# Kernel tuning notes

Hardware: AMD Instinct MI355X
Metric: run time of the kernel (lower is better)

The kernel has to match this reference:

```python
import jax, jax.numpy as jnp
import numpy as np
import math

# static config
NH, HD, HID = 16, 128, 2048
ROT = 64            # head_dim * partial_rotary_factor(0.5)
EPS = 1e-6
GROUPS = 8
CHUNK = 64
THETA = 10000.0
LAYER_IDX, N_LAYERS = 1, 32
B, S = 2, 2048


def _base_slopes(n):
    # power-of-two branch of HF ALiBi slopes
    start = 2 ** (-(2 ** (-(math.log2(n) - 3))))
    return [start * (start ** i) for i in range(n)]

# per-head log-decay (negative): slope = -base * (1 - (l-1)/(L-1) + 1e-5)
SLOPE = jnp.asarray(
    -np.array(_base_slopes(NH), dtype=np.float32)
    * (1.0 - (LAYER_IDX - 1) / (N_LAYERS - 1) + 1e-5),
    dtype=jnp.float32)  # [NH]


def _rmsnorm(x, w):
    return x * jax.lax.rsqrt(jnp.mean(x * x, axis=-1, keepdims=True) + EPS) * w


def _partial_rope(x, positions):
    # x: [B,S,NH,HD]; neox-style rotary on first ROT dims, rest passthrough
    half = ROT // 2
    inv_freq = 1.0 / (THETA ** (jnp.arange(half, dtype=jnp.float32) / half))
    ang = positions.astype(jnp.float32)[:, None] * inv_freq       # [S, half]
    cos = jnp.cos(ang)[None, :, None, :]
    sin = jnp.sin(ang)[None, :, None, :]
    x1, x2, rest = x[..., :half], x[..., half:ROT], x[..., ROT:]
    return jnp.concatenate(
        [x1 * cos - x2 * sin, x2 * cos + x1 * sin, rest], axis=-1)


def setup_inputs() -> dict:
    key = jax.random.key(0)
    ks = jax.random.split(key, 4)
    return {
        'positions': jnp.arange(S, dtype=jnp.int32),
        'hidden_states': jax.random.normal(ks[0], (B, S, HID), jnp.float32),
        'recurrent_state': jnp.zeros((B, NH, HD, HD), jnp.float32),
        'w_qkv': jax.random.normal(ks[1], (HID, 3 * NH * HD), jnp.float32) * 0.02,
        'w_g': jax.random.normal(ks[2], (HID, NH * HD), jnp.float32) * 0.02,
        'w_dense': jax.random.normal(ks[3], (NH * HD, HID), jnp.float32) * 0.02,
        'q_norm_w': jnp.ones((HD,), jnp.float32),
        'k_norm_w': jnp.ones((HD,), jnp.float32),
        'g_norm_w': jnp.ones((NH * HD,), jnp.float32),
    }


def reference(positions, hidden_states, recurrent_state, w_qkv, w_g, w_dense,
              q_norm_w, k_norm_w, g_norm_w):
    # fused QKV projection
    qkv = hidden_states @ w_qkv                       # [B,S,3*NH*HD]
    q, k, v = jnp.split(qkv, 3, axis=-1)
    q = q.reshape(B, S, NH, HD)
    k = k.reshape(B, S, NH, HD)
    v = v.reshape(B, S, NH, HD)

    # QK RMSNorm then partial rotary
    q = _partial_rope(_rmsnorm(q, q_norm_w), positions)
    k = _partial_rope(_rmsnorm(k, k_norm_w), positions)

    # chunked ALiBi-decayed linear attention:
    #   S_t = lam * S_{t-1} + k_t v_t^T ; o_t = q_t S_t, lam = exp(slope)
    NC = S // CHUNK
    qc = q.reshape(B, NC, CHUNK, NH, HD).transpose(1, 0, 3, 2, 4)  # [NC,B,NH,C,HD]
    kc = k.reshape(B, NC, CHUNK, NH, HD).transpose(1, 0, 3, 2, 4)
    vc = v.reshape(B, NC, CHUNK, NH, HD).transpose(1, 0, 3, 2, 4)

    t = jnp.arange(CHUNK, dtype=jnp.float32)
    # intra-chunk causal decay mask lam^(i-j), i>=j: [NH,C,C]
    dec_mask = jnp.where(t[:, None] >= t[None, :],
                         jnp.exp(SLOPE[:, None, None] * (t[:, None] - t[None, :])),
                         0.0)
    q_dec = jnp.exp(SLOPE[:, None] * (t[None, :] + 1.0))            # [NH,C] lam^(i+1)
    k_dec = jnp.exp(SLOPE[:, None] * (CHUNK - 1.0 - t[None, :]))    # [NH,C] lam^(C-1-j)
    lam_C = jnp.exp(SLOPE * CHUNK)                                   # [NH]

    def step(state, inp):
        qb, kb, vb = inp                                  # [B,NH,C,HD]
        scores = jnp.einsum('bhid,bhjd->bhij', qb, kb) * dec_mask[None]
        o_intra = jnp.einsum('bhij,bhjd->bhid', scores, vb)
        o_inter = jnp.einsum('bhid,bhde->bhie', qb * q_dec[None, :, :, None], state)
        new_state = (state * lam_C[None, :, None, None]
                     + jnp.einsum('bhjd,bhje->bhde', kb * k_dec[None, :, :, None], vb))
        return new_state, o_intra + o_inter

    _, o = jax.lax.scan(step, recurrent_state, (qc, kc, vc))  # o: [NC,B,NH,C,HD]
    o = o.transpose(1, 0, 3, 2, 4).reshape(B, S, NH * HD)

    # GroupRMSNorm on attention output, sigmoid gate, output projection
    og = o.reshape(B, S, GROUPS, (NH * HD) // GROUPS)
    og = og * jax.lax.rsqrt(jnp.mean(og * og, axis=-1, keepdims=True) + EPS)
    o = og.reshape(B, S, NH * HD) * g_norm_w
    o = o * jax.nn.sigmoid(hidden_states @ w_g)
    return o @ w_dense
```

## Files before the change

kernel.cpp:

```cpp
#include <hip/hip_runtime.h>
#include <hip/hip_bf16.h>
#include <math.h>

#define NH   16
#define HD   128
#define HID  2048
#define NKV  6144
#define B_   2
#define S_   2048
#define NC   32
#define CHUNK_ 64
#define GROUPS_ 8

typedef __bf16 bf16_t;
typedef bf16_t bf16x8 __attribute__((ext_vector_type(8)));
typedef float  f32x4  __attribute__((ext_vector_type(4)));

__device__ __forceinline__ float b2f(unsigned int u) {
    union { unsigned int u; float f; } c; c.u = (u & 0xffffu) << 16; return c.f;
}
__device__ __forceinline__ unsigned int f2b(float f) {
    union { float f; unsigned int u; } c; c.f = f;
    unsigned int u = c.u;
    return (u + 0x7fffu + ((u >> 16) & 1u)) >> 16;
}

#define GLOAD_LDS16(gp, lp) __builtin_amdgcn_global_load_lds(                     \
    (const __attribute__((address_space(1))) void*)(gp),                          \
    (__attribute__((address_space(3))) void*)(lp), 16, 0, 0)

__global__ __launch_bounds__(256) void cvt_bf16(const float* __restrict__ in,
                                                unsigned short* __restrict__ out, int n8)
{
    int i = blockIdx.x * 256 + threadIdx.x;
    if (i >= n8) return;
    const float4* p = (const float4*)in + (size_t)i * 2;
    float4 a = p[0], b = p[1];
    uint4 o;
    o.x = f2b(a.x) | (f2b(a.y) << 16);
    o.y = f2b(a.z) | (f2b(a.w) << 16);
    o.z = f2b(b.x) | (f2b(b.y) << 16);
    o.w = f2b(b.z) | (f2b(b.w) << 16);
    ((uint4*)out)[i] = o;
}

__global__ __launch_bounds__(256) void transpose_cvt(const float* __restrict__ in,
                                                     unsigned short* __restrict__ out,
                                                     int Kdim, int Ndim)
{
    __shared__ float tile[32][33];
    int ntx = Ndim >> 5;
    int bx = blockIdx.x % ntx;
    int by = blockIdx.x / ntx;
    int lx = threadIdx.x & 31, ly = threadIdx.x >> 5;
    int r0 = by * 32, c0 = bx * 32;
    #pragma unroll
    for (int r = 0; r < 4; ++r)
        tile[ly + r * 8][lx] = in[(size_t)(r0 + ly + r * 8) * Ndim + c0 + lx];
    __syncthreads();
    #pragma unroll
    for (int r = 0; r < 4; ++r)
        out[(size_t)(c0 + ly + r * 8) * Kdim + r0 + lx] = (unsigned short)f2b(tile[lx][ly + r * 8]);
}


__device__ __forceinline__ void ld_fr4(bf16x8 (&d)[4][2], const bf16_t* b, int s0, int ri) {
    #pragma unroll
    for (int i = 0; i < 4; ++i)
        #pragma unroll
        for (int k = 0; k < 2; ++k)
            d[i][k] = *(const bf16x8*)(b + (((s0 + i) * 2 + k) << 9) + ri);
}
__device__ __forceinline__ void ld_fr2(bf16x8 (&d)[2][2], const bf16_t* b, int s0, int ri) {
    #pragma unroll
    for (int i = 0; i < 2; ++i)
        #pragma unroll
        for (int k = 0; k < 2; ++k)
            d[i][k] = *(const bf16x8*)(b + (((s0 + i) * 2 + k) << 9) + ri);
}
__device__ __forceinline__ void mfma_quad(f32x4 (&a)[4][2], const bf16x8 (&af)[4][2],
                                          const bf16x8 (&bv)[2][2]) {
    #pragma unroll
    for (int mt = 0; mt < 4; ++mt)
        #pragma unroll
        for (int nt = 0; nt < 2; ++nt)
            #pragma unroll
            for (int ks = 0; ks < 2; ++ks)
                a[mt][nt] = __builtin_amdgcn_mfma_f32_16x16x32_bf16(af[mt][ks], bv[nt][ks], a[mt][nt], 0, 0, 0);
}

#define BAR()     asm volatile("s_barrier" ::: "memory")
#define VMCNT0()  asm volatile("s_waitcnt vmcnt(0)" ::: "memory")

__global__ __launch_bounds__(512, 2) void gemm_qg_256(const bf16_t* __restrict__ A,
                                                      const bf16_t* __restrict__ Bt,
                                                      unsigned short* __restrict__ Cq,
                                                      unsigned short* __restrict__ Cg)
{
    __shared__ bf16_t Asm[2][2][8192];
    __shared__ bf16_t Bsm[2][2][8192];
    const int K  = HID;
    const int NT = K / 64;

    int tid  = threadIdx.x;
    int wave = tid >> 6, lane = tid & 63;
    int wm = wave >> 2, wn = wave & 3;
    int l16 = lane & 15, quad = lane >> 4;
    int wm4 = wm * 4, wn2 = wn * 2;

    int bid = blockIdx.x;
    int xcd = bid & 7, idx = bid >> 3;
    int by  = (xcd >> 2) * 8 + (idx >> 3);
    int bx  = (xcd & 3) * 8 + (idx & 7);

    int rd_in = ((l16 << 5) | (quad << 3)) ^ (((l16 >> 3) & 1) << 4);

    int ch = lane ^ ((lane & 32) >> 4);
    int rr = ch >> 2;
    int cc = (ch & 3) * 8;

    const bf16_t* aSrc0 = A  + (size_t)(by * 256 +       wave * 16 + rr) * K + cc;
    const bf16_t* aSrc1 = A  + (size_t)(by * 256 + 128 + wave * 16 + rr) * K + cc;
    const bf16_t* bSrc0 = Bt + (size_t)(bx * 256 +       wave * 16 + rr) * K + cc;
    const bf16_t* bSrc1 = Bt + (size_t)(bx * 256 + 128 + wave * 16 + rr) * K + cc;

#define STAGE_A(h, t) do {                                                        \
        const bf16_t* _g = ((h) ? aSrc1 : aSrc0) + (size_t)(t) * 64;              \
        bf16_t* _l = &Asm[(t) & 1][(h)][wave * 1024 + lane * 8];                  \
        GLOAD_LDS16(_g,      _l);                                                 \
        GLOAD_LDS16(_g + 32, _l + 512); } while (0)
#define STAGE_B(h, t) do {                                                        \
        const bf16_t* _g = ((h) ? bSrc1 : bSrc0) + (size_t)(t) * 64;              \
        bf16_t* _l = &Bsm[(t) & 1][(h)][wave * 1024 + lane * 8];                  \
        GLOAD_LDS16(_g,      _l);                                                 \
        GLOAD_LDS16(_g + 32, _l + 512); } while (0)

    f32x4 acc[2][2][4][2];
    #pragma unroll
    for (int a0 = 0; a0 < 2; ++a0)
        #pragma unroll
        for (int a1 = 0; a1 < 2; ++a1)
            #pragma unroll
            for (int a2 = 0; a2 < 4; ++a2)
                #pragma unroll
                for (int a3 = 0; a3 < 2; ++a3) { f32x4 z = {0.f,0.f,0.f,0.f}; acc[a0][a1][a2][a3] = z; }

    STAGE_A(0, 0); STAGE_B(0, 0); STAGE_A(1, 0); STAGE_B(1, 0);
    VMCNT0();
    BAR();

    #pragma unroll 2
    for (int t = 0; t < NT - 1; ++t) {
        const int buf = t & 1;
        STAGE_A(0, t + 1); STAGE_B(0, t + 1); STAGE_A(1, t + 1); STAGE_B(1, t + 1);
        {
            bf16x8 afA[4][2], afB[4][2], bf0[2][2], bf1[2][2];
            ld_fr4(afA, &Asm[buf][0][0], wm4, rd_in);
            ld_fr2(bf0, &Bsm[buf][0][0], wn2, rd_in);
            mfma_quad(acc[0][0], afA, bf0);
            ld_fr2(bf1, &Bsm[buf][1][0], wn2, rd_in);
            mfma_quad(acc[0][1], afA, bf1);
            ld_fr4(afB, &Asm[buf][1][0], wm4, rd_in);
            mfma_quad(acc[1][1], afB, bf1);
            mfma_quad(acc[1][0], afB, bf0);
        }
        VMCNT0();
        BAR();
    }
    {
        const int buf = (NT - 1) & 1;
        bf16x8 afA[4][2], afB[4][2], bf0[2][2], bf1[2][2];
        ld_fr4(afA, &Asm[buf][0][0], wm4, rd_in);
        ld_fr2(bf0, &Bsm[buf][0][0], wn2, rd_in);
        mfma_quad(acc[0][0], afA, bf0);
        ld_fr2(bf1, &Bsm[buf][1][0], wn2, rd_in);
        mfma_quad(acc[0][1], afA, bf1);
        ld_fr4(afB, &Asm[buf][1][0], wm4, rd_in);
        mfma_quad(acc[1][1], afB, bf1);
        mfma_quad(acc[1][0], afB, bf0);
    }
#undef STAGE_A
#undef STAGE_B

    unsigned short* Cc; int Nn, colbase;
    if (bx < 24) { Cc = Cq; Nn = NKV; colbase = bx * 256; }
    else         { Cc = Cg; Nn = HID; colbase = bx * 256 - NKV; }
    int row0 = by * 256 + wm * 64 + quad * 4;
    int col0 = colbase + wn * 32 + l16;
    #pragma unroll
    for (int mh = 0; mh < 2; ++mh)
        #pragma unroll
        for (int nh = 0; nh < 2; ++nh)
            #pragma unroll
            for (int mt = 0; mt < 4; ++mt)
                #pragma unroll
                for (int nt = 0; nt < 2; ++nt) {
                    int col = col0 + nh * 128 + nt * 16;
                    #pragma unroll
                    for (int r = 0; r < 4; ++r) {
                        int row = row0 + mh * 128 + mt * 16 + r;
                        Cc[(size_t)row * Nn + col] = (unsigned short)f2b(acc[mh][nh][mt][nt][r]);
                    }
                }
}

__global__ __launch_bounds__(256, 2) void gemm_out_128(const bf16_t* __restrict__ A,
                                                       const bf16_t* __restrict__ Bt,
                                                       float* __restrict__ C)
{
    __shared__ bf16_t As[2][4096];
    __shared__ bf16_t Bs[2][4096];
    const int K  = HID;
    const int NT = K / 32;

    int tid  = threadIdx.x;
    int wave = tid >> 6, lane = tid & 63;
    int wm2 = wave >> 1, wn2 = wave & 1;
    int l16 = lane & 15, quad = lane >> 4;
    int w2 = wave * 2;

    int bid = blockIdx.x;
    int xcd = bid & 7, idx = bid >> 3;
    int by  = (xcd >> 1) * 8 + (idx >> 3);
    int bx  = (xcd & 1) * 8 + (idx & 7);

    int rd_in = ((l16 << 5) | (quad << 3)) ^ (((l16 >> 3) & 1) << 4);
    int ch = lane ^ ((lane & 32) >> 4);
    int rr = ch >> 2;
    int cc = (ch & 3) * 8;

    const bf16_t* aSrc = A  + (size_t)(by * 128 + w2 * 16 + rr) * K + cc;
    const bf16_t* bSrc = Bt + (size_t)(bx * 128 + w2 * 16 + rr) * K + cc;

#define OSTAGE(t) do {                                                            \
        const int nb_ = (t) & 1;                                                  \
        const bf16_t* _ga = aSrc + (size_t)(t) * 32;                              \
        const bf16_t* _gb = bSrc + (size_t)(t) * 32;                              \
        GLOAD_LDS16(_ga,                  &As[nb_][w2 * 512 + lane * 8]);         \
        GLOAD_LDS16(_ga + (size_t)16 * K, &As[nb_][w2 * 512 + 512 + lane * 8]);   \
        GLOAD_LDS16(_gb,                  &Bs[nb_][w2 * 512 + lane * 8]);         \
        GLOAD_LDS16(_gb + (size_t)16 * K, &Bs[nb_][w2 * 512 + 512 + lane * 8]); } while (0)

    f32x4 acc[4][4];
    #pragma unroll
    for (int i = 0; i < 4; ++i)
        #pragma unroll
        for (int j = 0; j < 4; ++j) { f32x4 z = {0.f,0.f,0.f,0.f}; acc[i][j] = z; }

#define OCOMP(t) do {                                                             \
        const int b_ = (t) & 1;                                                   \
        bf16x8 af_[4], bf_[4];                                                    \
        _Pragma("unroll")                                                         \
        for (int i = 0; i < 4; ++i)                                               \
            af_[i] = *(const bf16x8*)(&As[b_][((wm2 * 4 + i) << 9) + rd_in]);     \
        _Pragma("unroll")                                                         \
        for (int j = 0; j < 4; ++j)                                               \
            bf_[j] = *(const bf16x8*)(&Bs[b_][((wn2 * 4 + j) << 9) + rd_in]);     \
        _Pragma("unroll")                                                         \
        for (int i = 0; i < 4; ++i)                                               \
            _Pragma("unroll")                                                     \
            for (int j = 0; j < 4; ++j)                                           \
                acc[i][j] = __builtin_amdgcn_mfma_f32_16x16x32_bf16(af_[i], bf_[j], acc[i][j], 0, 0, 0); } while (0)

    OSTAGE(0);
    VMCNT0();
    BAR();
    #pragma unroll 2
    for (int t = 0; t < NT - 1; ++t) {
        OSTAGE(t + 1);
        OCOMP(t);
        VMCNT0();
        BAR();
    }
    OCOMP(NT - 1);
#undef OSTAGE
#undef OCOMP

    #pragma unroll
    for (int i = 0; i < 4; ++i)
        #pragma unroll
        for (int j = 0; j < 4; ++j) {
            int col = bx * 128 + wn2 * 64 + j * 16 + l16;
            #pragma unroll
            for (int r = 0; r < 4; ++r) {
                int row = by * 128 + wm2 * 64 + i * 16 + quad * 4 + r;
                C[(size_t)row * HID + col] = acc[i][j][r];
            }
        }
}

__global__ __launch_bounds__(256) void norm_rope(unsigned short* __restrict__ qkv,
                                                 const int* __restrict__ positions,
                                                 const float* __restrict__ qw,
                                                 const float* __restrict__ kw)
{
    int bs = blockIdx.x;
    int s  = bs & (S_ - 1);
    int tid = threadIdx.x;
    int l16 = tid & 15;
    unsigned short* base = qkv + (size_t)bs * NKV;
    float pos = (float)positions[s];

    #pragma unroll
    for (int p = 0; p < 2; ++p) {
        int rr = p * 16 + (tid >> 4);
        int qk = rr >> 4;
        int h  = rr & 15;
        unsigned short* row = base + qk * HID + h * HD;
        const float* w = qk ? kw : qw;
        uint4 v = *(const uint4*)(row + l16 * 8);
        float x[8];
        x[0] = b2f(v.x); x[1] = b2f(v.x >> 16);
        x[2] = b2f(v.y); x[3] = b2f(v.y >> 16);
        x[4] = b2f(v.z); x[5] = b2f(v.z >> 16);
        x[6] = b2f(v.w); x[7] = b2f(v.w >> 16);
        float ss = 0.f;
        #pragma unroll
        for (int t = 0; t < 8; ++t) ss += x[t] * x[t];
        ss += __shfl_xor(ss, 1); ss += __shfl_xor(ss, 2);
        ss += __shfl_xor(ss, 4); ss += __shfl_xor(ss, 8);
        float inv = rsqrtf(ss * (1.0f / 128.0f) + 1e-6f);
        float n[8];
        #pragma unroll
        for (int t = 0; t < 8; ++t) n[t] = x[t] * inv * w[l16 * 8 + t];
        float pr[8];
        #pragma unroll
        for (int t = 0; t < 8; ++t) pr[t] = __shfl_xor(n[t], 4);
        if (l16 < 8) {
            #pragma unroll
            for (int t = 0; t < 8; ++t) {
                int dim = l16 * 8 + t;
                int i = dim & 31;
                float ang = pos * exp2f(-(float)i * 0.4152410118609203f);
                float cs = cosf(ang), sn = sinf(ang);
                n[t] = (dim < 32) ? (n[t] * cs - pr[t] * sn) : (n[t] * cs + pr[t] * sn);
            }
        }
        uint4 o;
        o.x = f2b(n[0]) | (f2b(n[1]) << 16);
        o.y = f2b(n[2]) | (f2b(n[3]) << 16);
        o.z = f2b(n[4]) | (f2b(n[5]) << 16);
        o.w = f2b(n[6]) | (f2b(n[7]) << 16);
        *(uint4*)(row + l16 * 8) = o;
    }
}

__global__ __launch_bounds__(256) void chunk_kv(const unsigned short* __restrict__ qkv,
                                                unsigned short* __restrict__ wbuf)
{
    __shared__ unsigned short kt[128 * 72];
    __shared__ unsigned short vt[128 * 72];
    int bi = blockIdx.x;
    int c = bi & 31, bh = bi >> 5, h = bh & 15, b = bh >> 4;
    int tid = threadIdx.x;
    float slope = -exp2f(-0.5f * (float)(h + 1)) * (1.0f + 1e-5f);

    const unsigned short* kbase = qkv + ((size_t)(b * S_ + c * CHUNK_)) * NKV + HID + h * HD;
    const unsigned short* vbase = kbase + HID;

    for (int idx = tid; idx < 4096; idx += 256) {
        int j = idx >> 6, p = idx & 63;
        unsigned int ku = *(const unsigned int*)(kbase + (size_t)j * NKV + p * 2);
        kt[(2 * p) * 72 + j]     = (unsigned short)(ku & 0xffffu);
        kt[(2 * p + 1) * 72 + j] = (unsigned short)(ku >> 16);
        float kd = expf(slope * (float)(63 - j));
        unsigned int vu = *(const unsigned int*)(vbase + (size_t)j * NKV + p * 2);
        vt[(2 * p) * 72 + j]     = (unsigned short)f2b(b2f(vu) * kd);
        vt[(2 * p + 1) * 72 + j] = (unsigned short)f2b(b2f(vu >> 16) * kd);
    }
    __syncthreads();

    int lane = tid & 63, wave = tid >> 6;
    int wm = (wave >> 1) * 64;
    int wn = (wave & 1) * 64;
    int l16 = lane & 15, quad = lane >> 4;

    f32x4 acc[4][4];
    #pragma unroll
    for (int i = 0; i < 4; ++i)
        #pragma unroll
        for (int j = 0; j < 4; ++j) { f32x4 z = {0.f,0.f,0.f,0.f}; acc[i][j] = z; }

    #pragma unroll
    for (int ks = 0; ks < 64; ks += 32) {
        bf16x8 af[4], bf[4];
        #pragma unroll
        for (int t = 0; t < 4; ++t) {
            af[t] = *(const bf16x8*)((const bf16_t*)vt + (wm + t * 16 + l16) * 72 + ks + quad * 8);
            bf[t] = *(const bf16x8*)((const bf16_t*)kt + (wn + t * 16 + l16) * 72 + ks + quad * 8);
        }
        #pragma unroll
        for (int mt = 0; mt < 4; ++mt)
            #pragma unroll
            for (int nt = 0; nt < 4; ++nt)
                acc[mt][nt] = __builtin_amdgcn_mfma_f32_16x16x32_bf16(af[mt], bf[nt], acc[mt][nt], 0, 0, 0);
    }

    unsigned short* wp = wbuf + ((size_t)bi << 14);
    #pragma unroll
    for (int mt = 0; mt < 4; ++mt)
        #pragma unroll
        for (int nt = 0; nt < 4; ++nt) {
            int dcol = wn + nt * 16 + l16;
            #pragma unroll
            for (int r = 0; r < 4; ++r) {
                int erow = wm + mt * 16 + quad * 4 + r;
                wp[(size_t)erow * 128 + dcol] = (unsigned short)f2b(acc[mt][nt][r]);
            }
        }
}

__global__ __launch_bounds__(256) void state_scan(const unsigned short* __restrict__ wbuf,
                                                  const float* __restrict__ rs0,
                                                  unsigned short* __restrict__ stbuf)
{
    int bi = blockIdx.x;
    int es = bi & 15, bh = bi >> 4, h = bh & 15, b = bh >> 4;
    int tid = threadIdx.x;
    float slope = -exp2f(-0.5f * (float)(h + 1)) * (1.0f + 1e-5f);
    float lam = expf(slope * 64.0f);

    int e  = es * 8 + (tid >> 5);
    int d0 = (tid & 31) * 4;

    float S[4];
    const float* rp = rs0 + ((size_t)(b * NH + h)) * HD * HD + e;
    #pragma unroll
    for (int t = 0; t < 4; ++t) S[t] = rp[(size_t)(d0 + t) * HD];

    size_t off = (size_t)e * 128 + d0;
    size_t base = (((size_t)bh * NC) << 14) + off;
    uint2 w0 = *(const uint2*)(wbuf + base);
    uint2 w1 = *(const uint2*)(wbuf + base + (1 << 14));
    for (int c = 0; c < NC; ++c) {
        uint2 o;
        o.x = f2b(S[0]) | (f2b(S[1]) << 16);
        o.y = f2b(S[2]) | (f2b(S[3]) << 16);
        *(uint2*)(stbuf + base) = o;
        uint2 w2 = w1;
        if (c + 2 < NC) w2 = *(const uint2*)(wbuf + base + (2 << 14));
        S[0] = S[0] * lam + b2f(w0.x);
        S[1] = S[1] * lam + b2f(w0.x >> 16);
        S[2] = S[2] * lam + b2f(w0.y);
        S[3] = S[3] * lam + b2f(w0.y >> 16);
        w0 = w1; w1 = w2;
        base += (1 << 14);
    }
}

__global__ __launch_bounds__(256) void chunk_out(const unsigned short* __restrict__ qkv,
                                                 const unsigned short* __restrict__ stbuf,
                                                 unsigned short* __restrict__ obuf)
{
    __shared__ unsigned short qs[64 * 136];
    __shared__ unsigned short kss[64 * 136];
    __shared__ unsigned short vt[128 * 72];
    __shared__ unsigned short sc[64 * 72];

    int bi = blockIdx.x;
    int c = bi & 31, bh = bi >> 5, h = bh & 15, b = bh >> 4;
    int tid = threadIdx.x;
    float slope = -exp2f(-0.5f * (float)(h + 1)) * (1.0f + 1e-5f);

    int lane = tid & 63, wave = tid >> 6;
    int l16 = lane & 15, quad = lane >> 4;
    int wn3 = wave * 32;

    const unsigned short* stp = stbuf + (((size_t)bh * NC + c) << 14);
    bf16x8 bsf[4][2];
    #pragma unroll
    for (int ksp4 = 0; ksp4 < 4; ++ksp4)
        #pragma unroll
        for (int nt = 0; nt < 2; ++nt)
            bsf[ksp4][nt] = *(const bf16x8*)((const bf16_t*)stp +
                (size_t)(wn3 + nt * 16 + l16) * 128 + ksp4 * 32 + quad * 8);

    const unsigned short* qrow = qkv + ((size_t)(b * S_ + c * CHUNK_)) * NKV + h * HD;
    const unsigned short* krow = qrow + HID;
    for (int idx = tid; idx < 1024; idx += 256) {
        int row = idx >> 4, c8 = (idx & 15) * 8;
        *(uint4*)(qs  + row * 136 + c8) = *(const uint4*)(qrow + (size_t)row * NKV + c8);
        *(uint4*)(kss + row * 136 + c8) = *(const uint4*)(krow + (size_t)row * NKV + c8);
    }
    const unsigned short* vbase = qrow + 2 * HID;
    for (int idx = tid; idx < 4096; idx += 256) {
        int j = idx >> 6, p = idx & 63;
        unsigned int vu = *(const unsigned int*)(vbase + (size_t)j * NKV + p * 2);
        vt[(2 * p) * 72 + j]     = (unsigned short)(vu & 0xffffu);
        vt[(2 * p + 1) * 72 + j] = (unsigned short)(vu >> 16);
    }
    __syncthreads();

    {
        f32x4 accS[4];
        #pragma unroll
        for (int t = 0; t < 4; ++t) { f32x4 z = {0.f,0.f,0.f,0.f}; accS[t] = z; }
        #pragma unroll
        for (int ksp = 0; ksp < 128; ksp += 32) {
            bf16x8 aq = *(const bf16x8*)((const bf16_t*)qs + (wave * 16 + l16) * 136 + ksp + quad * 8);
            #pragma unroll
            for (int nt = 0; nt < 4; ++nt) {
                bf16x8 bk = *(const bf16x8*)((const bf16_t*)kss + (nt * 16 + l16) * 136 + ksp + quad * 8);
                accS[nt] = __builtin_amdgcn_mfma_f32_16x16x32_bf16(aq, bk, accS[nt], 0, 0, 0);
            }
        }
        float ad[4];
        #pragma unroll
        for (int r = 0; r < 4; ++r) ad[r] = expf(slope * (float)(wave * 16 + quad * 4 + r));
        #pragma unroll
        for (int nt = 0; nt < 4; ++nt) {
            int j = nt * 16 + l16;
            float bd = expf(-slope * (float)j);
            #pragma unroll
            for (int r = 0; r < 4; ++r) {
                int i = wave * 16 + quad * 4 + r;
                float v = (i >= j) ? accS[nt][r] * ad[r] * bd : 0.0f;
                sc[i * 72 + j] = (unsigned short)f2b(v);
            }
        }
    }
    __syncthreads();

    f32x4 accI[4][2], accE[4][2];
    #pragma unroll
    for (int i = 0; i < 4; ++i)
        #pragma unroll
        for (int j = 0; j < 2; ++j) { f32x4 z = {0.f,0.f,0.f,0.f}; accI[i][j] = z; accE[i][j] = z; }

    #pragma unroll
    for (int ksp = 0; ksp < 64; ksp += 32) {
        bf16x8 as[4], bv[2];
        #pragma unroll
        for (int mt = 0; mt < 4; ++mt)
            as[mt] = *(const bf16x8*)((const bf16_t*)sc + (mt * 16 + l16) * 72 + ksp + quad * 8);
        #pragma unroll
        for (int nt = 0; nt < 2; ++nt)
            bv[nt] = *(const bf16x8*)((const bf16_t*)vt + (wn3 + nt * 16 + l16) * 72 + ksp + quad * 8);
        #pragma unroll
        for (int mt = 0; mt < 4; ++mt)
            #pragma unroll
            for (int nt = 0; nt < 2; ++nt)
                accI[mt][nt] = __builtin_amdgcn_mfma_f32_16x16x32_bf16(as[mt], bv[nt], accI[mt][nt], 0, 0, 0);
    }
    #pragma unroll
    for (int ksp4 = 0; ksp4 < 4; ++ksp4) {
        bf16x8 aq[4];
        #pragma unroll
        for (int mt = 0; mt < 4; ++mt)
            aq[mt] = *(const bf16x8*)((const bf16_t*)qs + (mt * 16 + l16) * 136 + ksp4 * 32 + quad * 8);
        #pragma unroll
        for (int mt = 0; mt < 4; ++mt)
            #pragma unroll
            for (int nt = 0; nt < 2; ++nt)
                accE[mt][nt] = __builtin_amdgcn_mfma_f32_16x16x32_bf16(aq[mt], bsf[ksp4][nt], accE[mt][nt], 0, 0, 0);
    }

    #pragma unroll
    for (int mt = 0; mt < 4; ++mt) {
        #pragma unroll
        for (int r = 0; r < 4; ++r) {
            int i = mt * 16 + quad * 4 + r;
            float qd = expf(slope * (float)(i + 1));
            int orow = b * S_ + c * CHUNK_ + i;
            #pragma unroll
            for (int nt = 0; nt < 2; ++nt) {
                int col = h * HD + wn3 + nt * 16 + l16;
                float o = accI[mt][nt][r] + qd * accE[mt][nt][r];
                obuf[(size_t)orow * 2048 + col] = (unsigned short)f2b(o);
            }
        }
    }
}

__global__ __launch_bounds__(256) void gnorm_gate(const unsigned short* __restrict__ o,
                                                  unsigned short* __restrict__ gate,
                                                  const float* __restrict__ gw)
{
    int row = blockIdx.x >> 3;
    int g   = blockIdx.x & 7;
    int col = g * 256 + threadIdx.x;
    size_t idx = (size_t)row * 2048 + col;
    float ov = b2f(o[idx]);
    float ss = ov * ov;
    #pragma unroll
    for (int off = 32; off > 0; off >>= 1) ss += __shfl_xor(ss, off);
    __shared__ float part[4];
    if ((threadIdx.x & 63) == 0) part[threadIdx.x >> 6] = ss;
    __syncthreads();
    float tot = part[0] + part[1] + part[2] + part[3];
    float inv = rsqrtf(tot * (1.0f / 256.0f) + 1e-6f);
    float gv = b2f(gate[idx]);
    float sig = 1.0f / (1.0f + expf(-gv));
    gate[idx] = (unsigned short)f2b(ov * inv * gw[col] * sig);
}

extern "C" void kernel_launch(void* const* d_in, const int* in_sizes, int n_in,
                              void* d_out, int out_size, void* d_ws, size_t ws_size,
                              hipStream_t stream) {
    const int*   positions = (const int*)d_in[0];
    const float* hidden    = (const float*)d_in[1];
    const float* rstate    = (const float*)d_in[2];
    const float* w_qkv     = (const float*)d_in[3];
    const float* w_g       = (const float*)d_in[4];
    const float* w_dense   = (const float*)d_in[5];
    const float* q_norm_w  = (const float*)d_in[6];
    const float* k_norm_w  = (const float*)d_in[7];
    const float* g_norm_w  = (const float*)d_in[8];
    float* out = (float*)d_out;

    const int MR = B_ * S_;

    char* w = (char*)d_ws;
    unsigned short* qkv  = (unsigned short*)w;            w += (size_t)MR * NKV * 2;
    unsigned short* gbuf = (unsigned short*)w;            w += (size_t)MR * 2048 * 2;
    unsigned short* wdT  = (unsigned short*)w;            w += (size_t)HID * HID * 2;
    char* regionA = w;                                    w += (size_t)MR * HID * 2 + (size_t)8192 * HID * 2;
    char* regionB = w;
    unsigned short* hbf   = (unsigned short*)regionA;
    unsigned short* btQG  = (unsigned short*)(regionA + (size_t)MR * HID * 2);
    unsigned short* wqT   = btQG;
    unsigned short* wgT   = btQG + (size_t)NKV * HID;
    unsigned short* stbuf = (unsigned short*)regionA;
    unsigned short* wbuf  = (unsigned short*)regionB;
    unsigned short* obuf  = (unsigned short*)regionB;

    cvt_bf16<<<dim3((MR * HID / 8 + 255) / 256), dim3(256), 0, stream>>>(hidden, hbf, MR * HID / 8);
    transpose_cvt<<<dim3((HID / 32) * (NKV / 32)), dim3(256), 0, stream>>>(w_qkv, wqT, HID, NKV);
    transpose_cvt<<<dim3((HID / 32) * (HID / 32)), dim3(256), 0, stream>>>(w_g, wgT, HID, HID);
    transpose_cvt<<<dim3((HID / 32) * (HID / 32)), dim3(256), 0, stream>>>(w_dense, wdT, HID, HID);

    gemm_qg_256<<<dim3(512), dim3(512), 0, stream>>>(
        (const bf16_t*)hbf, (const bf16_t*)btQG, qkv, gbuf);
    norm_rope<<<dim3(B_ * S_), dim3(256), 0, stream>>>(qkv, positions, q_norm_w, k_norm_w);

    chunk_kv<<<dim3(B_ * NH * NC), dim3(256), 0, stream>>>(qkv, wbuf);
    state_scan<<<dim3(B_ * NH * 16), dim3(256), 0, stream>>>(wbuf, rstate, stbuf);
    chunk_out<<<dim3(B_ * NH * NC), dim3(256), 0, stream>>>(qkv, stbuf, obuf);

    gnorm_gate<<<dim3(MR * GROUPS_), dim3(256), 0, stream>>>(obuf, gbuf, g_norm_w);
    gemm_out_128<<<dim3(512), dim3(256), 0, stream>>>(
        (const bf16_t*)gbuf, (const bf16_t*)wdT, out);
}
```

Before: 424.1 us.

## Retile QG GEMM to 128x256, fragment-native state layout, vectorize scan and gnorm

The QKV/gate GEMM drops from 256x256 tiles with 512 threads to 128x256 tiles with 256 threads, K-step 32, launched over 1024 blocks. The state buffer is now written in MFMA-fragment order so chunk_out can read B fragments with contiguous per-lane loads. state_scan is changed to 8-element vectors to match. gnorm_gate now handles one full row per block with 8 bf16 values per thread and reduces with wave shuffles. These changes aim to cut GEMM tail and occupancy costs and uncoalesced memory access, at the price of lower per-block reuse in the GEMM and a layout that must agree across three kernels.

Result: slower. 435.6 us (+2.7%).

```diff
diff --git a/kernel.cpp b/kernel.cpp
--- a/kernel.cpp
+++ b/kernel.cpp
@@ -28,6 +28,9 @@
 #define GLOAD_LDS16(gp, lp) __builtin_amdgcn_global_load_lds(                     \
     (const __attribute__((address_space(1))) void*)(gp),                          \
     (__attribute__((address_space(3))) void*)(lp), 16, 0, 0)
+
+#define BAR()     asm volatile("s_barrier" ::: "memory")
+#define VMCNT0()  asm volatile("s_waitcnt vmcnt(0)" ::: "memory")
 
 __global__ __launch_bounds__(256) void cvt_bf16(const float* __restrict__ in,
                                                 unsigned short* __restrict__ out, int n8)
@@ -63,145 +66,93 @@
         out[(size_t)(c0 + ly + r * 8) * Kdim + r0 + lx] = (unsigned short)f2b(tile[lx][ly + r * 8]);
 }
 
-
-__device__ __forceinline__ void ld_fr4(bf16x8 (&d)[4][2], const bf16_t* b, int s0, int ri) {
-    #pragma unroll
-    for (int i = 0; i < 4; ++i)
-        #pragma unroll
-        for (int k = 0; k < 2; ++k)
-            d[i][k] = *(const bf16x8*)(b + (((s0 + i) * 2 + k) << 9) + ri);
-}
-__device__ __forceinline__ void ld_fr2(bf16x8 (&d)[2][2], const bf16_t* b, int s0, int ri) {
-    #pragma unroll
-    for (int i = 0; i < 2; ++i)
-        #pragma unroll
-        for (int k = 0; k < 2; ++k)
-            d[i][k] = *(const bf16x8*)(b + (((s0 + i) * 2 + k) << 9) + ri);
-}
-__device__ __forceinline__ void mfma_quad(f32x4 (&a)[4][2], const bf16x8 (&af)[4][2],
-                                          const bf16x8 (&bv)[2][2]) {
-    #pragma unroll
-    for (int mt = 0; mt < 4; ++mt)
-        #pragma unroll
-        for (int nt = 0; nt < 2; ++nt)
-            #pragma unroll
-            for (int ks = 0; ks < 2; ++ks)
-                a[mt][nt] = __builtin_amdgcn_mfma_f32_16x16x32_bf16(af[mt][ks], bv[nt][ks], a[mt][nt], 0, 0, 0);
-}
-
-#define BAR()     asm volatile("s_barrier" ::: "memory")
-#define VMCNT0()  asm volatile("s_waitcnt vmcnt(0)" ::: "memory")
-
-__global__ __launch_bounds__(512, 2) void gemm_qg_256(const bf16_t* __restrict__ A,
+__global__ __launch_bounds__(256, 2) void gemm_qg_128(const bf16_t* __restrict__ A,
                                                       const bf16_t* __restrict__ Bt,
                                                       unsigned short* __restrict__ Cq,
                                                       unsigned short* __restrict__ Cg)
 {
-    __shared__ bf16_t Asm[2][2][8192];
-    __shared__ bf16_t Bsm[2][2][8192];
+    __shared__ bf16_t Asm[2][4096];
+    __shared__ bf16_t Bsm[2][8192];
     const int K  = HID;
-    const int NT = K / 64;
+    const int NT = K / 32;
 
     int tid  = threadIdx.x;
     int wave = tid >> 6, lane = tid & 63;
-    int wm = wave >> 2, wn = wave & 3;
     int l16 = lane & 15, quad = lane >> 4;
-    int wm4 = wm * 4, wn2 = wn * 2;
 
     int bid = blockIdx.x;
     int xcd = bid & 7, idx = bid >> 3;
-    int by  = (xcd >> 2) * 8 + (idx >> 3);
-    int bx  = (xcd & 3) * 8 + (idx & 7);
+    int by  = (xcd >> 1) * 8 + (idx >> 4);
+    int bx  = (xcd & 1) * 16 + (idx & 15);
 
     int rd_in = ((l16 << 5) | (quad << 3)) ^ (((l16 >> 3) & 1) << 4);
-
     int ch = lane ^ ((lane & 32) >> 4);
     int rr = ch >> 2;
     int cc = (ch & 3) * 8;
 
-    const bf16_t* aSrc0 = A  + (size_t)(by * 256 +       wave * 16 + rr) * K + cc;
-    const bf16_t* aSrc1 = A  + (size_t)(by * 256 + 128 + wave * 16 + rr) * K + cc;
-    const bf16_t* bSrc0 = Bt + (size_t)(bx * 256 +       wave * 16 + rr) * K + cc;
-    const bf16_t* bSrc1 = Bt + (size_t)(bx * 256 + 128 + wave * 16 + rr) * K + cc;
-
-#define STAGE_A(h, t) do {                                                        \
-        const bf16_t* _g = ((h) ? aSrc1 : aSrc0) + (size_t)(t) * 64;              \
-        bf16_t* _l = &Asm[(t) & 1][(h)][wave * 1024 + lane * 8];                  \
-        GLOAD_LDS16(_g,      _l);                                                 \
-        GLOAD_LDS16(_g + 32, _l + 512); } while (0)
-#define STAGE_B(h, t) do {                                                        \
-        const bf16_t* _g = ((h) ? bSrc1 : bSrc0) + (size_t)(t) * 64;              \
-        bf16_t* _l = &Bsm[(t) & 1][(h)][wave * 1024 + lane * 8];                  \
-        GLOAD_LDS16(_g,      _l);                                                 \
-        GLOAD_LDS16(_g + 32, _l + 512); } while (0)
-
-    f32x4 acc[2][2][4][2];
-    #pragma unroll
-    for (int a0 = 0; a0 < 2; ++a0)
-        #pragma unroll
-        for (int a1 = 0; a1 < 2; ++a1)
-            #pragma unroll
-            for (int a2 = 0; a2 < 4; ++a2)
-                #pragma unroll
-                for (int a3 = 0; a3 < 2; ++a3) { f32x4 z = {0.f,0.f,0.f,0.f}; acc[a0][a1][a2][a3] = z; }
-
-    STAGE_A(0, 0); STAGE_B(0, 0); STAGE_A(1, 0); STAGE_B(1, 0);
+    const bf16_t* aSrc = A  + (size_t)(by * 128 + wave * 32 + rr) * K + cc;
+    const bf16_t* bSrc = Bt + (size_t)(bx * 256 + wave * 64 + rr) * K + cc;
+
+#define QSTAGE(t) do {                                                            \
+        const int nb_ = (t) & 1;                                                  \
+        const bf16_t* _ga = aSrc + (size_t)(t) * 32;                              \
+        const bf16_t* _gb = bSrc + (size_t)(t) * 32;                              \
+        GLOAD_LDS16(_ga,                  &Asm[nb_][(2*wave  )*512 + lane*8]);    \
+        GLOAD_LDS16(_ga + (size_t)16 * K, &Asm[nb_][(2*wave+1)*512 + lane*8]);    \
+        GLOAD_LDS16(_gb,                  &Bsm[nb_][(4*wave  )*512 + lane*8]);    \
+        GLOAD_LDS16(_gb + (size_t)16 * K, &Bsm[nb_][(4*wave+1)*512 + lane*8]);    \
+        GLOAD_LDS16(_gb + (size_t)32 * K, &Bsm[nb_][(4*wave+2)*512 + lane*8]);    \
+        GLOAD_LDS16(_gb + (size_t)48 * K, &Bsm[nb_][(4*wave+3)*512 + lane*8]); } while (0)
+
+    f32x4 acc[8][4];
+    #pragma unroll
+    for (int i = 0; i < 8; ++i)
+        #pragma unroll
+        for (int j = 0; j < 4; ++j) { f32x4 z = {0.f,0.f,0.f,0.f}; acc[i][j] = z; }
+
+#define QCOMP(t) do {                                                             \
+        const int b_ = (t) & 1;                                                   \
+        bf16x8 af_[8], bf_[4];                                                    \
+        _Pragma("unroll")                                                         \
+        for (int j = 0; j < 4; ++j)                                               \
+            bf_[j] = *(const bf16x8*)(&Bsm[b_][((wave*4 + j) << 9) + rd_in]);     \
+        _Pragma("unroll")                                                         \
+        for (int i = 0; i < 8; ++i)                                               \
+            af_[i] = *(const bf16x8*)(&Asm[b_][(i << 9) + rd_in]);                \
+        _Pragma("unroll")                                                         \
+        for (int i = 0; i < 8; ++i)                                               \
+            _Pragma("unroll")                                                     \
+            for (int j = 0; j < 4; ++j)                                           \
+                acc[i][j] = __builtin_amdgcn_mfma_f32_16x16x32_bf16(af_[i], bf_[j], acc[i][j], 0, 0, 0); } while (0)
+
+    QSTAGE(0);
     VMCNT0();
     BAR();
-
     #pragma unroll 2
     for (int t = 0; t < NT - 1; ++t) {
-        const int buf = t & 1;
-        STAGE_A(0, t + 1); STAGE_B(0, t + 1); STAGE_A(1, t + 1); STAGE_B(1, t + 1);
-        {
-            bf16x8 afA[4][2], afB[4][2], bf0[2][2], bf1[2][2];
-            ld_fr4(afA, &Asm[buf][0][0], wm4, rd_in);
-            ld_fr2(bf0, &Bsm[buf][0][0], wn2, rd_in);
-            mfma_quad(acc[0][0], afA, bf0);
-            ld_fr2(bf1, &Bsm[buf][1][0], wn2, rd_in);
-            mfma_quad(acc[0][1], afA, bf1);
-            ld_fr4(afB, &Asm[buf][1][0], wm4, rd_in);
-            mfma_quad(acc[1][1], afB, bf1);
-            mfma_quad(acc[1][0], afB, bf0);
-        }
+        QSTAGE(t + 1);
+        QCOMP(t);
         VMCNT0();
         BAR();
     }
-    {
-        const int buf = (NT - 1) & 1;
-        bf16x8 afA[4][2], afB[4][2], bf0[2][2], bf1[2][2];
-        ld_fr4(afA, &Asm[buf][0][0], wm4, rd_in);
-        ld_fr2(bf0, &Bsm[buf][0][0], wn2, rd_in);
-        mfma_quad(acc[0][0], afA, bf0);
-        ld_fr2(bf1, &Bsm[buf][1][0], wn2, rd_in);
-        mfma_quad(acc[0][1], afA, bf1);
-        ld_fr4(afB, &Asm[buf][1][0], wm4, rd_in);
-        mfma_quad(acc[1][1], afB, bf1);
-        mfma_quad(acc[1][0], afB, bf0);
-    }
-#undef STAGE_A
-#undef STAGE_B
+    QCOMP(NT - 1);
+#undef QSTAGE
+#undef QCOMP
 
     unsigned short* Cc; int Nn, colbase;
     if (bx < 24) { Cc = Cq; Nn = NKV; colbase = bx * 256; }
     else         { Cc = Cg; Nn = HID; colbase = bx * 256 - NKV; }
-    int row0 = by * 256 + wm * 64 + quad * 4;
-    int col0 = colbase + wn * 32 + l16;
-    #pragma unroll
-    for (int mh = 0; mh < 2; ++mh)
-        #pragma unroll
-        for (int nh = 0; nh < 2; ++nh)
-            #pragma unroll
-            for (int mt = 0; mt < 4; ++mt)
-                #pragma unroll
-                for (int nt = 0; nt < 2; ++nt) {
-                    int col = col0 + nh * 128 + nt * 16;
-                    #pragma unroll
-                    for (int r = 0; r < 4; ++r) {
-                        int row = row0 + mh * 128 + mt * 16 + r;
-                        Cc[(size_t)row * Nn + col] = (unsigned short)f2b(acc[mh][nh][mt][nt][r]);
-                    }
-                }
+    #pragma unroll
+    for (int i = 0; i < 8; ++i)
+        #pragma unroll
+        for (int j = 0; j < 4; ++j) {
+            int col = colbase + wave * 64 + j * 16 + l16;
+            #pragma unroll
+            for (int r = 0; r < 4; ++r) {
+                int row = by * 128 + i * 16 + quad * 4 + r;
+                Cc[(size_t)row * Nn + col] = (unsigned short)f2b(acc[i][j][r]);
+            }
+        }
 }
 
 __global__ __launch_bounds__(256, 2) void gemm_out_128(const bf16_t* __restrict__ A,
@@ -401,11 +352,12 @@
     for (int mt = 0; mt < 4; ++mt)
         #pragma unroll
         for (int nt = 0; nt < 4; ++nt) {
-            int dcol = wn + nt * 16 + l16;
+            int cid = ((wave >> 1) * 4 + mt) * 4 + (wave & 1) * 2 + (nt >> 1);
+            int pos = ((nt & 1) * 2 + (l16 >> 3)) * 128 + (l16 & 7);
             #pragma unroll
             for (int r = 0; r < 4; ++r) {
-                int erow = wm + mt * 16 + quad * 4 + r;
-                wp[(size_t)erow * 128 + dcol] = (unsigned short)f2b(acc[mt][nt][r]);
+                int e15 = quad * 4 + r;
+                wp[cid * 512 + pos + e15 * 8] = (unsigned short)f2b(acc[mt][nt][r]);
             }
         }
 }
@@ -415,34 +367,37 @@
                                                   unsigned short* __restrict__ stbuf)
 {
     int bi = blockIdx.x;
-    int es = bi & 15, bh = bi >> 4, h = bh & 15, b = bh >> 4;
+    int s = bi & 7, bh = bi >> 3, h = bh & 15, b = bh >> 4;
     int tid = threadIdx.x;
     float slope = -exp2f(-0.5f * (float)(h + 1)) * (1.0f + 1e-5f);
     float lam = expf(slope * 64.0f);
 
-    int e  = es * 8 + (tid >> 5);
-    int d0 = (tid & 31) * 4;
-
-    float S[4];
+    int T  = s * 256 + tid;
+    int cid = T >> 6, lc = T & 63;
+    int e  = (cid >> 2) * 16 + (lc & 15);
+    int d0 = (cid & 3) * 32 + (lc >> 4) * 8;
+
+    float S[8];
     const float* rp = rs0 + ((size_t)(b * NH + h)) * HD * HD + e;
     #pragma unroll
-    for (int t = 0; t < 4; ++t) S[t] = rp[(size_t)(d0 + t) * HD];
-
-    size_t off = (size_t)e * 128 + d0;
-    size_t base = (((size_t)bh * NC) << 14) + off;
-    uint2 w0 = *(const uint2*)(wbuf + base);
-    uint2 w1 = *(const uint2*)(wbuf + base + (1 << 14));
+    for (int t = 0; t < 8; ++t) S[t] = rp[(size_t)(d0 + t) * HD];
+
+    size_t base = (((size_t)bh * NC) << 14) + (size_t)T * 8;
+    uint4 w0 = *(const uint4*)(wbuf + base);
+    uint4 w1 = *(const uint4*)(wbuf + base + (1 << 14));
     for (int c = 0; c < NC; ++c) {
-        uint2 o;
+        uint4 o;
         o.x = f2b(S[0]) | (f2b(S[1]) << 16);
         o.y = f2b(S[2]) | (f2b(S[3]) << 16);
-        *(uint2*)(stbuf + base) = o;
-        uint2 w2 = w1;
-        if (c + 2 < NC) w2 = *(const uint2*)(wbuf + base + (2 << 14));
-        S[0] = S[0] * lam + b2f(w0.x);
-        S[1] = S[1] * lam + b2f(w0.x >> 16);
-        S[2] = S[2] * lam + b2f(w0.y);
-        S[3] = S[3] * lam + b2f(w0.y >> 16);
+        o.z = f2b(S[4]) | (f2b(S[5]) << 16);
+        o.w = f2b(S[6]) | (f2b(S[7]) << 16);
+        *(uint4*)(stbuf + base) = o;
+        uint4 w2 = w1;
+        if (c + 2 < NC) w2 = *(const uint4*)(wbuf + base + (2 << 14));
+        S[0] = S[0] * lam + b2f(w0.x); S[1] = S[1] * lam + b2f(w0.x >> 16);
+        S[2] = S[2] * lam + b2f(w0.y); S[3] = S[3] * lam + b2f(w0.y >> 16);
+        S[4] = S[4] * lam + b2f(w0.z); S[5] = S[5] * lam + b2f(w0.z >> 16);
+        S[6] = S[6] * lam + b2f(w0.w); S[7] = S[7] * lam + b2f(w0.w >> 16);
         w0 = w1; w1 = w2;
         base += (1 << 14);
     }
@@ -473,7 +428,7 @@
         #pragma unroll
         for (int nt = 0; nt < 2; ++nt)
             bsf[ksp4][nt] = *(const bf16x8*)((const bf16_t*)stp +
-                (size_t)(wn3 + nt * 16 + l16) * 128 + ksp4 * 32 + quad * 8);
+                (((wave * 2 + nt) * 4 + ksp4) << 9) + lane * 8);
 
     const unsigned short* qrow = qkv + ((size_t)(b * S_ + c * CHUNK_)) * NKV + h * HD;
     const unsigned short* krow = qrow + HID;
@@ -576,22 +531,42 @@
                                                   unsigned short* __restrict__ gate,
                                                   const float* __restrict__ gw)
 {
-    int row = blockIdx.x >> 3;
-    int g   = blockIdx.x & 7;
-    int col = g * 256 + threadIdx.x;
-    size_t idx = (size_t)row * 2048 + col;
-    float ov = b2f(o[idx]);
-    float ss = ov * ov;
-    #pragma unroll
-    for (int off = 32; off > 0; off >>= 1) ss += __shfl_xor(ss, off);
-    __shared__ float part[4];
-    if ((threadIdx.x & 63) == 0) part[threadIdx.x >> 6] = ss;
-    __syncthreads();
-    float tot = part[0] + part[1] + part[2] + part[3];
-    float inv = rsqrtf(tot * (1.0f / 256.0f) + 1e-6f);
-    float gv = b2f(gate[idx]);
-    float sig = 1.0f / (1.0f + expf(-gv));
-    gate[idx] = (unsigned short)f2b(ov * inv * gw[col] * sig);
+    int row = blockIdx.x;
+    int tid = threadIdx.x;
+    size_t base8 = (size_t)row * 256 + tid;
+    uint4 ov = ((const uint4*)o)[base8];
+    uint4 gv = ((const uint4*)gate)[base8];
+    float x[8];
+    x[0] = b2f(ov.x); x[1] = b2f(ov.x >> 16);
+    x[2] = b2f(ov.y); x[3] = b2f(ov.y >> 16);
+    x[4] = b2f(ov.z); x[5] = b2f(ov.z >> 16);
+    x[6] = b2f(ov.w); x[7] = b2f(ov.w >> 16);
+    float ss = 0.f;
+    #pragma unroll
+    for (int t = 0; t < 8; ++t) ss += x[t] * x[t];
+    ss += __shfl_xor(ss, 1); ss += __shfl_xor(ss, 2); ss += __shfl_xor(ss, 4);
+    ss += __shfl_xor(ss, 8); ss += __shfl_xor(ss, 16);
+    float inv = rsqrtf(ss * (1.0f / 256.0f) + 1e-6f);
+    const float4* gwp = (const float4*)(gw + tid * 8);
+    float4 w0 = gwp[0], w1 = gwp[1];
+    float g[8];
+    g[0] = b2f(gv.x); g[1] = b2f(gv.x >> 16);
+    g[2] = b2f(gv.y); g[3] = b2f(gv.y >> 16);
+    g[4] = b2f(gv.z); g[5] = b2f(gv.z >> 16);
+    g[6] = b2f(gv.w); g[7] = b2f(gv.w >> 16);
+    float wv[8] = {w0.x, w0.y, w0.z, w0.w, w1.x, w1.y, w1.z, w1.w};
+    float r[8];
+    #pragma unroll
+    for (int t = 0; t < 8; ++t) {
+        float sig = 1.0f / (1.0f + expf(-g[t]));
+        r[t] = x[t] * inv * wv[t] * sig;
+    }
+    uint4 out;
+    out.x = f2b(r[0]) | (f2b(r[1]) << 16);
+    out.y = f2b(r[2]) | (f2b(r[3]) << 16);
+    out.z = f2b(r[4]) | (f2b(r[5]) << 16);
+    out.w = f2b(r[6]) | (f2b(r[7]) << 16);
+    ((uint4*)gate)[base8] = out;
 }
 
 extern "C" void kernel_launch(void* const* d_in, const int* in_sizes, int n_in,
@@ -629,15 +604,15 @@
     transpose_cvt<<<dim3((HID / 32) * (HID / 32)), dim3(256), 0, stream>>>(w_g, wgT, HID, HID);
     transpose_cvt<<<dim3((HID / 32) * (HID / 32)), dim3(256), 0, stream>>>(w_dense, wdT, HID, HID);
 
-    gemm_qg_256<<<dim3(512), dim3(512), 0, stream>>>(
+    gemm_qg_128<<<dim3(1024), dim3(256), 0, stream>>>(
         (const bf16_t*)hbf, (const bf16_t*)btQG, qkv, gbuf);
     norm_rope<<<dim3(B_ * S_), dim3(256), 0, stream>>>(qkv, positions, q_norm_w, k_norm_w);
 
     chunk_kv<<<dim3(B_ * NH * NC), dim3(256), 0, stream>>>(qkv, wbuf);
-    state_scan<<<dim3(B_ * NH * 16), dim3(256), 0, stream>>>(wbuf, rstate, stbuf);
+    state_scan<<<dim3(B_ * NH * 8), dim3(256), 0, stream>>>(wbuf, rstate, stbuf);
     chunk_out<<<dim3(B_ * NH * NC), dim3(256), 0, stream>>>(qkv, stbuf, obuf);
 
-    gnorm_gate<<<dim3(MR * GROUPS_), dim3(256), 0, stream>>>(obuf, gbuf, g_norm_w);
+    gnorm_gate<<<dim3(MR), dim3(256), 0, stream>>>(obuf, gbuf, g_norm_w);
     gemm_out_128<<<dim3(512), dim3(256), 0, stream>>>(
         (const bf16_t*)gbuf, (const bf16_t*)wdT, out);
 }
```
